# Kernel tuning notes

Measured on AMD Instinct MI355X. Metric: run time of the kernel, lower is better.

The kernel has to match this reference:

```python
import jax, jax.numpy as jnp
import numpy as np

B, L, D = 64, 1024, 1024


def _attn(q, K, V, mask):
    # q: [B,D], K/V: [B,L,D], mask: [B,L] bool (True = valid)
    scores = jnp.einsum('bd,bld->bl', q, K) / jnp.sqrt(jnp.asarray(D, q.dtype))
    scores = jnp.where(mask, scores, -jnp.inf)
    attn = jax.nn.softmax(scores, axis=-1)
    attn = jnp.where(jnp.isnan(attn), 0.0, attn)  # torch.nan_to_num for all-masked rows
    return jnp.einsum('bl,bld->bd', attn, V)


def setup_inputs() -> dict:
    key = jax.random.key(0)
    ks = jax.random.split(key, 12)
    xav = float(np.sqrt(6.0 / (D + D)))  # xavier_uniform for square Linear
    img_mask = jax.random.randint(ks[4], (B, L), 0, 2).astype(bool)
    txt_mask = jax.random.randint(ks[7], (B, L), 0, 2).astype(bool)
    # guarantee at least one valid token per row
    img_mask = img_mask.at[:, 0].set(True)
    txt_mask = txt_mask.at[:, 0].set(True)
    return {
        'img_q': jax.random.normal(ks[0], (B, D), jnp.float32),
        'txt_q': jax.random.normal(ks[1], (B, D), jnp.float32),
        'K_img': jax.random.normal(ks[2], (B, L, D), jnp.float32),
        'V_img': jax.random.normal(ks[3], (B, L, D), jnp.float32),
        'img_mask': img_mask,
        'K_txt': jax.random.normal(ks[5], (B, L, D), jnp.float32),
        'V_txt': jax.random.normal(ks[6], (B, L, D), jnp.float32),
        'txt_mask': txt_mask,
        'W_img': jax.random.uniform(ks[8], (D, D), jnp.float32, -xav, xav),
        'b_img': jnp.zeros((D,), jnp.float32),
        'W_txt': jax.random.uniform(ks[9], (D, D), jnp.float32, -xav, xav),
        'b_txt': jnp.zeros((D,), jnp.float32),
    }


def reference(img_q, txt_q, K_img, V_img, img_mask, K_txt, V_txt, txt_mask,
              W_img, b_img, W_txt, b_txt):
    # Dropout is identity in eval mode.
    ctx_img = _attn(txt_q, K_img, V_img, img_mask)
    img_q = img_q + ctx_img @ W_img.T + b_img
    ctx_txt = _attn(img_q, K_txt, V_txt, txt_mask)
    txt_q = txt_q + ctx_txt @ W_txt.T + b_txt
    return (img_q, txt_q)
```

## Files before the change

kernel.cpp:

```cpp
#include <hip/hip_runtime.h>
#include <hip/hip_bf16.h>
#include <float.h>

#define B_ 64
#define L_ 1024
#define D_ 1024
#define NSPLIT 16
#define CHUNK 64
#define PSTRIDE 1028

typedef __bf16 bf16x8 __attribute__((ext_vector_type(8)));
typedef float f32x4 __attribute__((ext_vector_type(4)));

__device__ inline unsigned short f2bf(float x) {
    unsigned int u = __float_as_uint(x);
    unsigned int lsb = (u >> 16) & 1u;
    u += 0x7fffu + lsb;
    return (unsigned short)(u >> 16);
}

__global__ __launch_bounds__(256, 4) void attn_partial_kernel(
    const float* __restrict__ q,
    const float* __restrict__ K,
    const float* __restrict__ V,
    const int*   __restrict__ mask,
    float* __restrict__ part)
{
    const int bid  = blockIdx.x;
    const int b    = bid >> 4;
    const int sp   = bid & 15;
    const int l0   = sp * CHUNK;
    const int tid  = threadIdx.x;
    const int wave = tid >> 6;
    const int lane = tid & 63;

    __shared__ int   vidx[CHUNK];
    __shared__ float sc[CHUNK];
    __shared__ float pw[CHUNK];
    __shared__ int   nvalid;

    const float4* qptr = reinterpret_cast<const float4*>(q + (size_t)b * D_);
    float4 qreg[4];
    #pragma unroll
    for (int rep = 0; rep < 4; ++rep) qreg[rep] = qptr[lane + rep * 64];

    if (wave == 0) {
        int mv = mask[(size_t)b * L_ + l0 + lane];
        unsigned long long bal = __ballot(mv != 0);
        int nv   = __popcll(bal);
        int padv = bal ? (__ffsll((long long)bal) - 1) : 0;
        int rank = __popcll(bal & ((1ull << lane) - 1));
        if (mv) vidx[rank] = lane;
        if (lane >= nv) vidx[lane] = padv;
        if (lane == 0) nvalid = nv;
    }
    __syncthreads();
    const int nv  = nvalid;
    const int nvp = (nv + 7) & ~7;

    const float* Kb = K + ((size_t)b * L_ + l0) * D_;
    for (int jj = wave; jj < nvp; jj += 8) {
        int j2 = jj + 4;
        const float4* k0 = reinterpret_cast<const float4*>(Kb + (size_t)vidx[jj] * D_);
        const float4* k1 = reinterpret_cast<const float4*>(Kb + (size_t)vidx[j2] * D_);
        float a0 = 0.f, a1 = 0.f;
        float4 kv0[4], kv1[4];
        #pragma unroll
        for (int rep = 0; rep < 4; ++rep) { kv0[rep] = k0[lane + rep * 64];
                                            kv1[rep] = k1[lane + rep * 64]; }
        #pragma unroll
        for (int rep = 0; rep < 4; ++rep) {
            a0 += kv0[rep].x * qreg[rep].x + kv0[rep].y * qreg[rep].y
                + kv0[rep].z * qreg[rep].z + kv0[rep].w * qreg[rep].w;
            a1 += kv1[rep].x * qreg[rep].x + kv1[rep].y * qreg[rep].y
                + kv1[rep].z * qreg[rep].z + kv1[rep].w * qreg[rep].w;
        }
        #pragma unroll
        for (int off = 32; off > 0; off >>= 1) {
            a0 += __shfl_xor(a0, off, 64);
            a1 += __shfl_xor(a1, off, 64);
        }
        if (lane == 0) { sc[jj] = a0 * 0.03125f; sc[j2] = a1 * 0.03125f; }
    }
    __syncthreads();

    float m = -FLT_MAX;
    for (int j = 0; j < nv; ++j) m = fmaxf(m, sc[j]);

    if (tid < CHUNK) pw[tid] = (tid < nv) ? __expf(sc[tid] - m) : 0.f;
    __syncthreads();

    float se = 0.f;
    float ax = 0.f, ay = 0.f, az = 0.f, aw = 0.f;
    const float4* vbase = reinterpret_cast<const float4*>(V + ((size_t)b * L_ + l0) * D_);
    for (int j = 0; j < nvp; j += 8) {
        float p[8]; int ix[8];
        #pragma unroll
        for (int t = 0; t < 8; ++t) { p[t] = pw[j + t]; ix[t] = vidx[j + t]; }
        float4 vv[8];
        #pragma unroll
        for (int t = 0; t < 8; ++t) vv[t] = vbase[(size_t)ix[t] * (D_ / 4) + tid];
        #pragma unroll
        for (int t = 0; t < 8; ++t) {
            se += p[t];
            ax += p[t] * vv[t].x; ay += p[t] * vv[t].y;
            az += p[t] * vv[t].z; aw += p[t] * vv[t].w;
        }
    }

    float* po = part + (size_t)bid * PSTRIDE;
    float4 o; o.x = ax; o.y = ay; o.z = az; o.w = aw;
    reinterpret_cast<float4*>(po)[tid] = o;
    if (tid == 0) { po[D_] = m; po[D_ + 1] = se; }
}

__global__ __launch_bounds__(256) void combine_kernel(
    const float* __restrict__ part,
    unsigned short* __restrict__ ctxb)
{
    const int b   = blockIdx.x;
    const int tid = threadIdx.x;
    const float* pb = part + (size_t)b * NSPLIT * PSTRIDE;

    float ms[NSPLIT];
    float gm = -FLT_MAX;
    #pragma unroll
    for (int sp = 0; sp < NSPLIT; ++sp) {
        ms[sp] = pb[(size_t)sp * PSTRIDE + D_];
        gm = fmaxf(gm, ms[sp]);
    }
    float sca[NSPLIT];
    float denom = 0.f;
    #pragma unroll
    for (int sp = 0; sp < NSPLIT; ++sp) {
        float e = (ms[sp] == -FLT_MAX) ? 0.f : __expf(ms[sp] - gm);
        sca[sp] = e;
        denom += pb[(size_t)sp * PSTRIDE + D_ + 1] * e;
    }
    float inv = 1.f / denom;

    float ax = 0.f, ay = 0.f, az = 0.f, aw = 0.f;
    #pragma unroll
    for (int sp = 0; sp < NSPLIT; ++sp) {
        if (sca[sp] == 0.f) continue;
        float4 o = reinterpret_cast<const float4*>(pb + (size_t)sp * PSTRIDE)[tid];
        float s = sca[sp] * inv;
        ax += s * o.x; ay += s * o.y; az += s * o.z; aw += s * o.w;
    }
    ushort4 u;
    u.x = f2bf(ax); u.y = f2bf(ay); u.z = f2bf(az); u.w = f2bf(aw);
    reinterpret_cast<ushort4*>(ctxb)[(size_t)b * (D_ / 4) + tid] = u;
}

__global__ __launch_bounds__(256) void convert_kernel(
    const float* __restrict__ src, unsigned short* __restrict__ dst, int n4)
{
    int i = blockIdx.x * 256 + threadIdx.x;
    if (i >= n4) return;
    float4 v = reinterpret_cast<const float4*>(src)[i];
    ushort4 u;
    u.x = f2bf(v.x); u.y = f2bf(v.y); u.z = f2bf(v.z); u.w = f2bf(v.w);
    reinterpret_cast<ushort4*>(dst)[i] = u;
}

__global__ __launch_bounds__(256) void proj_kernel(
    const unsigned short* __restrict__ Abf,
    const unsigned short* __restrict__ Wbf,
    const float* __restrict__ qin,
    const float* __restrict__ bias,
    float* __restrict__ out)
{
    const int tid  = threadIdx.x;
    const int wave = tid >> 6;
    const int lane = tid & 63;
    const int m0   = (blockIdx.x & 3) * 16;
    const int n0   = (blockIdx.x >> 2) * 16;
    const int r    = lane & 15;
    const int g    = lane >> 4;

    const bf16x8* aptr = reinterpret_cast<const bf16x8*>(
        Abf + (size_t)(m0 + r) * D_ + g * 8 + wave * 256);
    const bf16x8* bptr = reinterpret_cast<const bf16x8*>(
        Wbf + (size_t)(n0 + r) * D_ + g * 8 + wave * 256);

    f32x4 acc = {0.f, 0.f, 0.f, 0.f};
    #pragma unroll
    for (int kk = 0; kk < 8; ++kk) {
        bf16x8 a  = aptr[kk * 4];
        bf16x8 bb = bptr[kk * 4];
        acc = __builtin_amdgcn_mfma_f32_16x16x32_bf16(a, bb, acc, 0, 0, 0);
    }

    __shared__ float red[1024];
    #pragma unroll
    for (int i = 0; i < 4; ++i) red[wave * 256 + lane * 4 + i] = acc[i];
    __syncthreads();

    int ol = tid >> 2, oi = tid & 3;
    float v = red[ol * 4 + oi] + red[256 + ol * 4 + oi]
            + red[512 + ol * 4 + oi] + red[768 + ol * 4 + oi];
    int row = m0 + ((ol >> 4) * 4 + oi);
    int col = n0 + (ol & 15);
    out[(size_t)row * D_ + col] = qin[(size_t)row * D_ + col] + bias[col] + v;
}

extern "C" void kernel_launch(void* const* d_in, const int* in_sizes, int n_in,
                              void* d_out, int out_size, void* d_ws, size_t ws_size,
                              hipStream_t stream) {
    const float* img_q    = (const float*)d_in[0];
    const float* txt_q    = (const float*)d_in[1];
    const float* K_img    = (const float*)d_in[2];
    const float* V_img    = (const float*)d_in[3];
    const int*   img_mask = (const int*)  d_in[4];
    const float* K_txt    = (const float*)d_in[5];
    const float* V_txt    = (const float*)d_in[6];
    const int*   txt_mask = (const int*)  d_in[7];
    const float* W_img    = (const float*)d_in[8];
    const float* b_img    = (const float*)d_in[9];
    const float* W_txt    = (const float*)d_in[10];
    const float* b_txt    = (const float*)d_in[11];

    float* out_img = (float*)d_out;
    float* out_txt = (float*)d_out + B_ * D_;

    char* ws = (char*)d_ws;
    float* part = (float*)ws;
    size_t part_bytes = (size_t)B_ * NSPLIT * PSTRIDE * sizeof(float);
    unsigned short* Wimg_bf = (unsigned short*)(ws + part_bytes);
    unsigned short* Wtxt_bf = Wimg_bf + (size_t)D_ * D_;
    unsigned short* ctx_bf  = Wtxt_bf + (size_t)D_ * D_;

    convert_kernel<<<1024, 256, 0, stream>>>(W_img, Wimg_bf, D_ * D_ / 4);
    convert_kernel<<<1024, 256, 0, stream>>>(W_txt, Wtxt_bf, D_ * D_ / 4);

    attn_partial_kernel<<<B_ * NSPLIT, 256, 0, stream>>>(txt_q, K_img, V_img, img_mask, part);
    combine_kernel<<<B_, 256, 0, stream>>>(part, ctx_bf);
    proj_kernel<<<256, 256, 0, stream>>>(ctx_bf, Wimg_bf, img_q, b_img, out_img);

    attn_partial_kernel<<<B_ * NSPLIT, 256, 0, stream>>>(out_img, K_txt, V_txt, txt_mask, part);
    combine_kernel<<<B_, 256, 0, stream>>>(part, ctx_bf);
    proj_kernel<<<256, 256, 0, stream>>>(ctx_bf, Wtxt_bf, txt_q, b_txt, out_txt);
}
```

Baseline: 139.9 us.

## Use larger chunks with 512-thread blocks in split-K attention and merge weight conversion

The attention partial kernel now splits each sequence into 8 chunks of 128 keys with 512-thread blocks instead of 16 chunks of 64 keys with 256 threads. Mask compaction now uses two ballots, the score max uses a wave shuffle reduction instead of a serial loop, the dot products use split accumulators, and each thread accumulates a float2 of V instead of a float4. The two weight-conversion launches are merged into one kernel. The intent is fewer partials for the combine step, less launch overhead and more memory-level parallelism per block, at the cost of fewer blocks in the grid.

```diff
diff --git a/kernel.cpp b/kernel.cpp
--- a/kernel.cpp
+++ b/kernel.cpp
@@ -5,8 +5,8 @@
 #define B_ 64
 #define L_ 1024
 #define D_ 1024
-#define NSPLIT 16
-#define CHUNK 64
+#define NSPLIT 8
+#define CHUNK 128
 #define PSTRIDE 1028
 
 typedef __bf16 bf16x8 __attribute__((ext_vector_type(8)));
@@ -19,7 +19,7 @@
     return (unsigned short)(u >> 16);
 }
 
-__global__ __launch_bounds__(256, 4) void attn_partial_kernel(
+__global__ __launch_bounds__(512, 4) void attn_partial_kernel(
     const float* __restrict__ q,
     const float* __restrict__ K,
     const float* __restrict__ V,
@@ -27,8 +27,8 @@
     float* __restrict__ part)
 {
     const int bid  = blockIdx.x;
-    const int b    = bid >> 4;
-    const int sp   = bid & 15;
+    const int b    = bid >> 3;
+    const int sp   = bid & 7;
     const int l0   = sp * CHUNK;
     const int tid  = threadIdx.x;
     const int wave = tid >> 6;
@@ -45,36 +45,48 @@
     for (int rep = 0; rep < 4; ++rep) qreg[rep] = qptr[lane + rep * 64];
 
     if (wave == 0) {
-        int mv = mask[(size_t)b * L_ + l0 + lane];
-        unsigned long long bal = __ballot(mv != 0);
-        int nv   = __popcll(bal);
-        int padv = bal ? (__ffsll((long long)bal) - 1) : 0;
-        int rank = __popcll(bal & ((1ull << lane) - 1));
-        if (mv) vidx[rank] = lane;
-        if (lane >= nv) vidx[lane] = padv;
+        const int* mp = mask + (size_t)b * L_ + l0;
+        int mv0 = mp[lane];
+        int mv1 = mp[64 + lane];
+        unsigned long long bal0 = __ballot(mv0 != 0);
+        unsigned long long bal1 = __ballot(mv1 != 0);
+        int n0 = __popcll(bal0);
+        int nv = n0 + __popcll(bal1);
+        unsigned long long lt = (1ull << lane) - 1;
+        if (mv0) vidx[__popcll(bal0 & lt)] = lane;
+        if (mv1) vidx[n0 + __popcll(bal1 & lt)] = 64 + lane;
+        int padv = bal0 ? (__ffsll((long long)bal0) - 1)
+                        : (bal1 ? 64 + __ffsll((long long)bal1) - 1 : 0);
+        if (nv + lane < CHUNK) vidx[nv + lane] = padv;
         if (lane == 0) nvalid = nv;
     }
     __syncthreads();
-    const int nv  = nvalid;
-    const int nvp = (nv + 7) & ~7;
+    const int nv    = nvalid;
+    const int nvp8  = (nv + 7)  & ~7;
+    const int nvp16 = (nv + 15) & ~15;
 
     const float* Kb = K + ((size_t)b * L_ + l0) * D_;
-    for (int jj = wave; jj < nvp; jj += 8) {
-        int j2 = jj + 4;
-        const float4* k0 = reinterpret_cast<const float4*>(Kb + (size_t)vidx[jj] * D_);
-        const float4* k1 = reinterpret_cast<const float4*>(Kb + (size_t)vidx[j2] * D_);
-        float a0 = 0.f, a1 = 0.f;
+    for (int jj = wave; jj < nvp16; jj += 16) {
+        int j2 = jj + 8;
+        const float4* k0 = reinterpret_cast<const float4*>(Kb + vidx[jj] * D_);
+        const float4* k1 = reinterpret_cast<const float4*>(Kb + vidx[j2] * D_);
         float4 kv0[4], kv1[4];
         #pragma unroll
         for (int rep = 0; rep < 4; ++rep) { kv0[rep] = k0[lane + rep * 64];
                                             kv1[rep] = k1[lane + rep * 64]; }
-        #pragma unroll
-        for (int rep = 0; rep < 4; ++rep) {
-            a0 += kv0[rep].x * qreg[rep].x + kv0[rep].y * qreg[rep].y
-                + kv0[rep].z * qreg[rep].z + kv0[rep].w * qreg[rep].w;
-            a1 += kv1[rep].x * qreg[rep].x + kv1[rep].y * qreg[rep].y
-                + kv1[rep].z * qreg[rep].z + kv1[rep].w * qreg[rep].w;
+        float a0a = 0.f, a0b = 0.f, a1a = 0.f, a1b = 0.f;
+        #pragma unroll
+        for (int rep = 0; rep < 4; rep += 2) {
+            a0a += kv0[rep].x * qreg[rep].x + kv0[rep].y * qreg[rep].y
+                 + kv0[rep].z * qreg[rep].z + kv0[rep].w * qreg[rep].w;
+            a0b += kv0[rep+1].x * qreg[rep+1].x + kv0[rep+1].y * qreg[rep+1].y
+                 + kv0[rep+1].z * qreg[rep+1].z + kv0[rep+1].w * qreg[rep+1].w;
+            a1a += kv1[rep].x * qreg[rep].x + kv1[rep].y * qreg[rep].y
+                 + kv1[rep].z * qreg[rep].z + kv1[rep].w * qreg[rep].w;
+            a1b += kv1[rep+1].x * qreg[rep+1].x + kv1[rep+1].y * qreg[rep+1].y
+                 + kv1[rep+1].z * qreg[rep+1].z + kv1[rep+1].w * qreg[rep+1].w;
         }
+        float a0 = a0a + a0b, a1 = a1a + a1b;
         #pragma unroll
         for (int off = 32; off > 0; off >>= 1) {
             a0 += __shfl_xor(a0, off, 64);
@@ -85,32 +97,33 @@
     __syncthreads();
 
     float m = -FLT_MAX;
-    for (int j = 0; j < nv; ++j) m = fmaxf(m, sc[j]);
+    if (lane < nv)      m = sc[lane];
+    if (lane + 64 < nv) m = fmaxf(m, sc[lane + 64]);
+    #pragma unroll
+    for (int off = 32; off > 0; off >>= 1) m = fmaxf(m, __shfl_xor(m, off, 64));
 
     if (tid < CHUNK) pw[tid] = (tid < nv) ? __expf(sc[tid] - m) : 0.f;
     __syncthreads();
 
-    float se = 0.f;
-    float ax = 0.f, ay = 0.f, az = 0.f, aw = 0.f;
-    const float4* vbase = reinterpret_cast<const float4*>(V + ((size_t)b * L_ + l0) * D_);
-    for (int j = 0; j < nvp; j += 8) {
+    float se = 0.f, ax = 0.f, ay = 0.f;
+    const float2* vbase = reinterpret_cast<const float2*>(V + ((size_t)b * L_ + l0) * D_);
+    for (int j = 0; j < nvp8; j += 8) {
         float p[8]; int ix[8];
         #pragma unroll
         for (int t = 0; t < 8; ++t) { p[t] = pw[j + t]; ix[t] = vidx[j + t]; }
-        float4 vv[8];
-        #pragma unroll
-        for (int t = 0; t < 8; ++t) vv[t] = vbase[(size_t)ix[t] * (D_ / 4) + tid];
+        float2 vv[8];
+        #pragma unroll
+        for (int t = 0; t < 8; ++t) vv[t] = vbase[ix[t] * (D_ / 2) + tid];
         #pragma unroll
         for (int t = 0; t < 8; ++t) {
             se += p[t];
             ax += p[t] * vv[t].x; ay += p[t] * vv[t].y;
-            az += p[t] * vv[t].z; aw += p[t] * vv[t].w;
         }
     }
 
     float* po = part + (size_t)bid * PSTRIDE;
-    float4 o; o.x = ax; o.y = ay; o.z = az; o.w = aw;
-    reinterpret_cast<float4*>(po)[tid] = o;
+    float2 o; o.x = ax; o.y = ay;
+    reinterpret_cast<float2*>(po)[tid] = o;
     if (tid == 0) { po[D_] = m; po[D_ + 1] = se; }
 }
 
@@ -152,15 +165,19 @@
     reinterpret_cast<ushort4*>(ctxb)[(size_t)b * (D_ / 4) + tid] = u;
 }
 
-__global__ __launch_bounds__(256) void convert_kernel(
-    const float* __restrict__ src, unsigned short* __restrict__ dst, int n4)
-{
+__global__ __launch_bounds__(256) void convert2_kernel(
+    const float* __restrict__ s0, const float* __restrict__ s1,
+    unsigned short* __restrict__ d0, unsigned short* __restrict__ d1)
+{
+    const int N4 = D_ * D_ / 4;
     int i = blockIdx.x * 256 + threadIdx.x;
-    if (i >= n4) return;
-    float4 v = reinterpret_cast<const float4*>(src)[i];
+    const float* s = (i < N4) ? s0 : s1;
+    unsigned short* d = (i < N4) ? d0 : d1;
+    int k = (i < N4) ? i : i - N4;
+    float4 v = reinterpret_cast<const float4*>(s)[k];
     ushort4 u;
     u.x = f2bf(v.x); u.y = f2bf(v.y); u.z = f2bf(v.z); u.w = f2bf(v.w);
-    reinterpret_cast<ushort4*>(dst)[i] = u;
+    reinterpret_cast<ushort4*>(d)[k] = u;
 }
 
 __global__ __launch_bounds__(256) void proj_kernel(
@@ -230,14 +247,13 @@
     unsigned short* Wtxt_bf = Wimg_bf + (size_t)D_ * D_;
     unsigned short* ctx_bf  = Wtxt_bf + (size_t)D_ * D_;
 
-    convert_kernel<<<1024, 256, 0, stream>>>(W_img, Wimg_bf, D_ * D_ / 4);
-    convert_kernel<<<1024, 256, 0, stream>>>(W_txt, Wtxt_bf, D_ * D_ / 4);
-
-    attn_partial_kernel<<<B_ * NSPLIT, 256, 0, stream>>>(txt_q, K_img, V_img, img_mask, part);
+    convert2_kernel<<<2048, 256, 0, stream>>>(W_img, W_txt, Wimg_bf, Wtxt_bf);
+
+    attn_partial_kernel<<<B_ * NSPLIT, 512, 0, stream>>>(txt_q, K_img, V_img, img_mask, part);
     combine_kernel<<<B_, 256, 0, stream>>>(part, ctx_bf);
     proj_kernel<<<256, 256, 0, stream>>>(ctx_bf, Wimg_bf, img_q, b_img, out_img);
 
-    attn_partial_kernel<<<B_ * NSPLIT, 256, 0, stream>>>(out_img, K_txt, V_txt, txt_mask, part);
+    attn_partial_kernel<<<B_ * NSPLIT, 512, 0, stream>>>(out_img, K_txt, V_txt, txt_mask, part);
     combine_kernel<<<B_, 256, 0, stream>>>(part, ctx_bf);
     proj_kernel<<<256, 256, 0, stream>>>(ctx_bf, Wtxt_bf, txt_q, b_txt, out_txt);
 }
```

Result: faster. 132.5 us (-5.3%).
